# Kernel tuning notes

Measured on AMD Instinct MI355X. Metric: run time of the kernel, lower is better.

Reference implementation:

```python
import jax, jax.numpy as jnp
import numpy as np
from jax import lax

N_TAPS = 27  # 3x3x3 kernel

def _gather_one(xb, ti, hi, wi):
    # xb: (C,T,H,W); ti/hi/wi: (T,H,W) int32. Zero-fill outside bounds.
    C, T, H, W = xb.shape
    valid = (ti >= 0) & (ti < T) & (hi >= 0) & (hi < H) & (wi >= 0) & (wi < W)
    lin = (jnp.clip(ti, 0, T - 1) * H + jnp.clip(hi, 0, H - 1)) * W + jnp.clip(wi, 0, W - 1)
    v = jnp.take(xb.reshape(C, -1), lin.reshape(-1), axis=1).reshape(C, T, H, W)
    return v * valid.astype(xb.dtype)

_gather = jax.vmap(_gather_one)  # over batch

def _trilinear(x, t, h, w):
    # x: (B,C,T,H,W); t/h/w: (B,T,H,W) float sample coordinates.
    t0, h0, w0 = jnp.floor(t), jnp.floor(h), jnp.floor(w)
    lt, lh, lw = t - t0, h - h0, w - w0
    t0i, h0i, w0i = t0.astype(jnp.int32), h0.astype(jnp.int32), w0.astype(jnp.int32)
    acc = 0.0
    for ti, wt in ((t0i, 1.0 - lt), (t0i + 1, lt)):
        for hi, wh in ((h0i, 1.0 - lh), (h0i + 1, lh)):
            for wi, ww in ((w0i, 1.0 - lw), (w0i + 1, lw)):
                acc = acc + _gather(x, ti, hi, wi) * (wt * wh * ww)[:, None]
    return acc  # (B,C,T,H,W)

def _deform_conv3d(x, offset_w, offset_b, weight):
    # x: (B,Cin,T,H,W). Offset layout: (B, 3, 27, T, H, W), axis1=(dt,dh,dw),
    # tap index k = kt*9 + kh*3 + kw. stride=1, padding=1, dilation=1, no bias.
    off = lax.conv_general_dilated(
        x, offset_w, (1, 1, 1), [(1, 1)] * 3,
        dimension_numbers=("NCDHW", "OIDHW", "NCDHW"))
    off = off + offset_b[None, :, None, None, None]
    B, _, T, H, W = off.shape
    off = off.reshape(B, 3, N_TAPS, T, H, W)
    tg = jnp.arange(T, dtype=x.dtype)[:, None, None]
    hg = jnp.arange(H, dtype=x.dtype)[None, :, None]
    wg = jnp.arange(W, dtype=x.dtype)[None, None, :]
    out = jnp.zeros((B, weight.shape[0], T, H, W), x.dtype)
    for k in range(N_TAPS):
        kt, kh, kw = k // 9, (k // 3) % 3, k % 3
        t = tg + (kt - 1) + off[:, 0, k]
        h = hg + (kh - 1) + off[:, 1, k]
        w = wg + (kw - 1) + off[:, 2, k]
        s = _trilinear(x, t, h, w)  # (B,Cin,T,H,W)
        out = out + jnp.einsum('bcthw,oc->bothw', s, weight[:, :, kt, kh, kw])
    return out

def setup_inputs() -> dict:
    key = jax.random.key(0)
    ks = jax.random.split(key, 4)
    B, T, C, H, W = 1, 4, 64, 128, 128
    x = jax.random.normal(ks[0], (B, T, C, H, W), jnp.float32)
    # small init scale keeps predicted offsets in a realistic +-2px range
    offset_w = jax.random.normal(ks[1], (3 * N_TAPS, C, 3, 3, 3), jnp.float32) * 0.02
    offset_b = jnp.zeros((3 * N_TAPS,), jnp.float32)
    weight = jax.random.normal(ks[2], (C, C, 3, 3, 3), jnp.float32) * 0.02
    gamma = jax.random.normal(ks[3], (1,), jnp.float32) * 0.1
    return {"x": x, "offset_w": offset_w, "offset_b": offset_b,
            "weight": weight, "gamma": gamma}

def reference(x, offset_w, offset_b, weight, gamma):
    xp = jnp.transpose(x, (0, 2, 1, 3, 4))  # (B,C,T,H,W)
    xc = _deform_conv3d(xp, offset_w, offset_b, weight)
    return gamma[0] * jnp.transpose(xc, (0, 2, 1, 3, 4)) + x
```

## Files before the change

kernel.cpp:

```cpp
#include <hip/hip_runtime.h>
#include <cmath>

#define Cc 64
#define Hh 128
#define Ww 128
#define HW_ 16384
#define THW_ 65536
#define CHW_ 1048576
#define NT 27

typedef unsigned short ushort_t;
typedef _Float16 f16x2 __attribute__((ext_vector_type(2)));
typedef _Float16 f16x8 __attribute__((ext_vector_type(8)));
typedef __fp16 fp16x2_alt __attribute__((ext_vector_type(2)));
typedef float floatx4 __attribute__((ext_vector_type(4)));
typedef unsigned uint4v __attribute__((ext_vector_type(4)));

union U32H2 { unsigned u; f16x2 h; };

static __device__ inline ushort_t f2h(float f) {
  union { _Float16 h; ushort_t u; } v;
  v.h = (_Float16)f;
  return v.u;
}

static __device__ inline unsigned pk2(float a) {
  union { fp16x2_alt h; unsigned u; } v;
  v.h = __builtin_amdgcn_cvt_pkrtz(a, a);
  return v.u;
}

static __device__ inline unsigned rep16(unsigned p) {
#if defined(__has_builtin)
#if __has_builtin(__builtin_amdgcn_perm)
  return __builtin_amdgcn_perm(p, p, 0x01000100u);
#else
  return (p & 0xFFFFu) * 0x10001u;
#endif
#else
  return (p & 0xFFFFu) * 0x10001u;
#endif
}

#if defined(__has_builtin)
#if __has_builtin(__builtin_amdgcn_make_buffer_rsrc) && __has_builtin(__builtin_amdgcn_raw_buffer_load_b32) && __has_builtin(__builtin_amdgcn_raw_buffer_load_b128)
#define USE_BUF 1
#endif
#endif
#ifndef USE_BUF
#define USE_BUF 0
#endif

struct XtBuf {
#if USE_BUF
  __amdgpu_buffer_rsrc_t r;
#else
  const char* p;
#endif
};

static __device__ inline XtBuf mkbuf(const ushort_t* xt) {
  XtBuf b;
#if USE_BUF
  b.r = __builtin_amdgcn_make_buffer_rsrc((void*)xt, (short)0, 8388608, 0x00020000);
#else
  b.p = (const char*)xt;
#endif
  return b;
}

static __device__ inline uint4v xload4(const XtBuf& b, unsigned voff) {
#if USE_BUF
  return __builtin_amdgcn_raw_buffer_load_b128(b.r, (int)voff, 0, 0);
#else
  return *(const uint4v*)(b.p + voff);
#endif
}


__global__ __launch_bounds__(256) void prep_transpose(
    const float* __restrict__ x, ushort_t* __restrict__ xt,
    const float* __restrict__ offset_w,
    const float* __restrict__ weight,
    ushort_t* __restrict__ w2frag,
    ushort_t* __restrict__ wfrag)
{
  __shared__ float tile[64][65];
  if (blockIdx.x < 1024) {
    int b = blockIdx.x;
    int wblk = b & 1;
    int th = b >> 1;
    int h = th & 127;
    int t = th >> 7;
    int w0 = wblk * 64;
    int lane = threadIdx.x & 63;
    int quad = threadIdx.x >> 6;
    #pragma unroll
    for (int cc = 0; cc < 16; ++cc) {
      int c = cc * 4 + quad;
      tile[c][lane] = x[t * CHW_ + c * HW_ + h * Ww + w0 + lane];
    }
    __syncthreads();
    #pragma unroll
    for (int ww = 0; ww < 16; ++ww) {
      int w = ww * 4 + quad;
      xt[(size_t)(t * HW_ + h * Ww + w0 + w) * 64 + lane] = f2h(tile[lane][w]);
    }
  } else {
    int e = (blockIdx.x - 1024) * 256 + threadIdx.x;
    if (e < 165888) {
      int j = e & 7, ln = (e >> 3) & 63, kh2 = (e >> 9) & 1, r = e >> 10;
      int ot = r % 6, k = r / 6;
      int oc = ot * 16 + (ln & 15);
      int c  = kh2 * 32 + (ln >> 4) * 8 + j;
      float v = (oc < 81) ? offset_w[(oc * 64 + c) * 27 + k] : 0.f;
      w2frag[e] = f2h(v);
    }
    if (e < 110592) {
      int j = e & 7, ln = (e >> 3) & 63, kh2 = (e >> 9) & 1, r = e >> 10;
      int ot = r & 3, k = r >> 2;
      int o = ot * 16 + (ln & 15);
      int c = kh2 * 32 + (ln >> 4) * 8 + j;
      wfrag[e] = f2h(weight[(o * 64 + c) * 27 + k]);
    }
  }
}

#define SITE(W, D, A0, A1, A2, A3) \
  { U32H2 wu; wu.u = (W); U32H2 q0, q1, q2, q3; \
    q0.u = (D)[0]; q1.u = (D)[1]; q2.u = (D)[2]; q3.u = (D)[3]; \
    A0 += wu.h * q0.h; A1 += wu.h * q1.h; A2 += wu.h * q2.h; A3 += wu.h * q3.h; }

__global__ __launch_bounds__(256, 3) void fused(
    const float* __restrict__ x,
    const ushort_t* __restrict__ xt,
    const ushort_t* __restrict__ w2frag,
    const float* __restrict__ ob,
    const ushort_t* __restrict__ wfrag,
    const float* __restrict__ gamma,
    float* __restrict__ out)
{
  __shared__ __align__(16) char lds[50768];
  ushort_t* S = (ushort_t*)lds;
  unsigned* pm0 = (unsigned*)(lds + 9216);
  unsigned* pm1 = (unsigned*)(lds + 11264);
  ushort_t* W2lds = (ushort_t*)(lds + 9216);
  ushort_t* Wl0 = (ushort_t*)(lds + 13312);
  ushort_t* Wl1 = (ushort_t*)(lds + 21504);
  float* Obuf = (float*)(lds + 29696);
  float* Dbuf = (float*)lds;
  int tid = threadIdx.x;
  int lane = tid & 63;
  int wavei = __builtin_amdgcn_readfirstlane(tid >> 6);
  int quad = lane >> 4;
  int m16 = lane & 15;
  int g8 = lane >> 3;
  unsigned coff = (unsigned)((lane & 7) * 16);
  int bid0 = blockIdx.x;
  int p0 = ((bid0 & 7) * 128 + (bid0 >> 3)) * 64;
  int t = p0 >> 14;
  int h = (p0 >> 7) & 127;
  int w0 = p0 & 127;
  XtBuf xb = mkbuf(xt);

  {
    floatx4 acc[6];
    #pragma unroll
    for (int i = 0; i < 6; ++i) acc[i] = (floatx4){0.f, 0.f, 0.f, 0.f};

    uint4v pd[2];
    uint4v w2reg[3];

    auto issue = [&](int k) {
      int kt = k / 9, kh = (k / 3) % 3, kw = k % 3;
      int ts = t + kt - 1, hs = h + kh - 1;
      int tsc = min(max(ts, 0), 3);
      int hsc = min(max(hs, 0), 127);
      int sbase = tsc * HW_ + hsc * Ww;
      #pragma unroll
      for (int b = 0; b < 2; ++b) {
        int prow = wavei * 16 + b * 8 + g8;
        int wc = w0 + prow + kw - 1;
        int wcc = min(max(wc, 0), 127);
        pd[b] = xload4(xb, ((unsigned)(sbase + wcc) << 7) + coff);
      }
    };
    auto wload = [&](int k) {
      const uint4v* src = (const uint4v*)(w2frag + (size_t)k * 6144);
      #pragma unroll
      for (int c = 0; c < 3; ++c) w2reg[c] = src[tid + c * 256];
    };
    auto wstore = [&]() {
      uint4v* dst = (uint4v*)W2lds;
      #pragma unroll
      for (int c = 0; c < 3; ++c) dst[tid + c * 256] = w2reg[c];
    };

    wload(0);
    wstore();
    __syncthreads();
    issue(0);

    #pragma unroll 1
    for (int k = 0; k < NT; ++k) {
      bool more = (k + 1 < NT);
      if (more) wload(k + 1);
      __builtin_amdgcn_sched_barrier(0);
      f16x8 wva[6], wvb[6];
      #pragma unroll
      for (int ot = 0; ot < 6; ++ot) {
        wva[ot] = *(const f16x8*)(W2lds + ot * 1024 + lane * 8);
        wvb[ot] = *(const f16x8*)(W2lds + ot * 1024 + 512 + lane * 8);
      }
      int kt = k / 9, kh = (k / 3) % 3, kw = k % 3;
      int ts = t + kt - 1, hs = h + kh - 1;
      bool rowok = ((unsigned)ts < 4u) && ((unsigned)hs < 128u);
      #pragma unroll
      for (int b = 0; b < 2; ++b) {
        int prow = wavei * 16 + b * 8 + g8;
        int wc = w0 + prow + kw - 1;
        bool ok = rowok && ((unsigned)wc < 128u);
        uint4v v = pd[b];
        if (!ok) v = (uint4v){0u, 0u, 0u, 0u};
        *(uint4v*)((char*)S + prow * 144 + coff) = v;
      }
      __builtin_amdgcn_sched_barrier(0);
      const ushort_t* srow = S + (wavei * 16 + m16) * 72 + quad * 8;
      f16x8 af0 = *(const f16x8*)srow;
      f16x8 af1 = *(const f16x8*)(srow + 32);
      #pragma unroll
      for (int ot = 0; ot < 6; ++ot) {
        acc[ot] = __builtin_amdgcn_mfma_f32_16x16x32_f16(af0, wva[ot], acc[ot], 0, 0, 0);
        acc[ot] = __builtin_amdgcn_mfma_f32_16x16x32_f16(af1, wvb[ot], acc[ot], 0, 0, 0);
      }
      __syncthreads();
      if (more) wstore();
      __syncthreads();
      if (more) issue(k + 1);
    }
    #pragma unroll
    for (int ot = 0; ot < 6; ++ot) {
      int oc = ot * 16 + m16;
      if (oc < 81) {
        float bv = ob[oc];
        #pragma unroll
        for (int r = 0; r < 4; ++r)
          Obuf[oc * 65 + wavei * 16 + quad * 4 + r] = acc[ot][r] + bv;
      }
    }
  }

  floatx4 acc[4];
  #pragma unroll
  for (int i = 0; i < 4; ++i) acc[i] = (floatx4){0.f, 0.f, 0.f, 0.f};

  int pl = wavei * 16 + m16;
  int aq = quad >> 1, bq = quad & 1;
  int rowA = wavei * 16 + g8;
  int rowB = rowA + 8;

  uint4v stage[16];
  uint4v wreg[2];

  auto meta = [&](int kk, float dtv, float dhv, float dwv) {
    unsigned* pm = (kk & 1) ? pm1 : pm0;
    int kt = kk / 9, kh = (kk / 3) % 3, kw = kk % 3;
    float tf = (float)(t + kt - 1) + dtv;
    float hf = (float)(h + kh - 1) + dhv;
    float wf = (float)(w0 + pl + kw - 1) + dwv;
    float tF = floorf(tf), hF = floorf(hf), wF = floorf(wf);
    float lt = tf - tF, lh_ = hf - hF, lw_ = wf - wF;
    int t0 = (int)tF, h0 = (int)hF, wq_ = (int)wF;
    int ti = t0 + aq;
    float wt_ = (aq ? lt : 1.f - lt) * (((unsigned)ti < 4u) ? 1.f : 0.f);
    int tic = min(max(ti, 0), 3);
    int hi = h0 + bq;
    float wh_ = (bq ? lh_ : 1.f - lh_) * (((unsigned)hi < 128u) ? 1.f : 0.f);
    int hic = min(max(hi, 0), 127);
    int base2 = tic * HW_ + hic * Ww;
    float bw = wt_ * wh_;
    int wi0 = wq_;
    float ww0 = (1.f - lw_) * (((unsigned)wi0 < 128u) ? 1.f : 0.f);
    int wi0c = min(max(wi0, 0), 127);
    int wi1 = wq_ + 1;
    float ww1 = lw_ * (((unsigned)wi1 < 128u) ? 1.f : 0.f);
    int wi1c = min(max(wi1, 0), 127);
    uint2 mp_;
    mp_.x = ((unsigned)(base2 + wi0c) << 16) | (pk2(bw * ww0) & 0xFFFFu);
    mp_.y = ((unsigned)(base2 + wi1c) << 16) | (pk2(bw * ww1) & 0xFFFFu);
    *(uint2*)&pm[pl * 8 + quad * 2] = mp_;
  };

  auto vof = [&](unsigned p) -> unsigned {
    return ((p >> 9) & 0xFFFFFF80u) + coff;
  };

  auto wload2 = [&](int k) {
    const uint4v* src = (const uint4v*)(wfrag + (size_t)k * 4096);
    wreg[0] = src[tid];
    wreg[1] = src[tid + 256];
  };
  auto wstore2 = [&](int k) {
    uint4v* dst = (uint4v*)((k & 1) ? Wl1 : Wl0);
    dst[tid] = wreg[0];
    dst[tid + 256] = wreg[1];
  };

  auto issueAll = [&](int kk) {
    const unsigned* pmn = (kk & 1) ? pm1 : pm0;
    const uint4* spA = (const uint4*)&pmn[rowA * 8];
    uint4 a0 = spA[0], a1 = spA[1];
    const uint4* spB = (const uint4*)&pmn[rowB * 8];
    uint4 b0 = spB[0], b1 = spB[1];
    stage[0]  = xload4(xb, vof(a0.x));
    stage[1]  = xload4(xb, vof(a0.y));
    stage[2]  = xload4(xb, vof(a0.z));
    stage[3]  = xload4(xb, vof(a0.w));
    stage[4]  = xload4(xb, vof(a1.x));
    stage[5]  = xload4(xb, vof(a1.y));
    stage[6]  = xload4(xb, vof(a1.z));
    stage[7]  = xload4(xb, vof(a1.w));
    stage[8]  = xload4(xb, vof(b0.x));
    stage[9]  = xload4(xb, vof(b0.y));
    stage[10] = xload4(xb, vof(b0.z));
    stage[11] = xload4(xb, vof(b0.w));
    stage[12] = xload4(xb, vof(b1.x));
    stage[13] = xload4(xb, vof(b1.y));
    stage[14] = xload4(xb, vof(b1.z));
    stage[15] = xload4(xb, vof(b1.w));
  };

  auto consumeA = [&](int kk) {
    const unsigned* pmc = (kk & 1) ? pm1 : pm0;
    const uint4* wp = (const uint4*)&pmc[rowA * 8];
    uint4 w03 = wp[0], w47 = wp[1];
    U32H2 z; z.u = 0;
    f16x2 e0 = z.h, e1 = z.h, e2 = z.h, e3 = z.h;
    f16x2 o0 = z.h, o1 = z.h, o2 = z.h, o3 = z.h;
    SITE(rep16(w03.x), stage[0], e0, e1, e2, e3)
    SITE(rep16(w03.y), stage[1], o0, o1, o2, o3)
    SITE(rep16(w03.z), stage[2], e0, e1, e2, e3)
    SITE(rep16(w03.w), stage[3], o0, o1, o2, o3)
    SITE(rep16(w47.x), stage[4], e0, e1, e2, e3)
    SITE(rep16(w47.y), stage[5], o0, o1, o2, o3)
    SITE(rep16(w47.z), stage[6], e0, e1, e2, e3)
    SITE(rep16(w47.w), stage[7], o0, o1, o2, o3)
    U32H2 r0, r1, r2, r3;
    r0.h = e0 + o0; r1.h = e1 + o1; r2.h = e2 + o2; r3.h = e3 + o3;
    uint4v res = {r0.u, r1.u, r2.u, r3.u};
    *(uint4v*)((char*)S + rowA * 144 + coff) = res;
  };
  auto consumeB = [&](int kk) {
    const unsigned* pmc = (kk & 1) ? pm1 : pm0;
    const uint4* wp = (const uint4*)&pmc[rowB * 8];
    uint4 w03 = wp[0], w47 = wp[1];
    U32H2 z; z.u = 0;
    f16x2 e0 = z.h, e1 = z.h, e2 = z.h, e3 = z.h;
    f16x2 o0 = z.h, o1 = z.h, o2 = z.h, o3 = z.h;
    SITE(rep16(w03.x), stage[8],  e0, e1, e2, e3)
    SITE(rep16(w03.y), stage[9],  o0, o1, o2, o3)
    SITE(rep16(w03.z), stage[10], e0, e1, e2, e3)
    SITE(rep16(w03.w), stage[11], o0, o1, o2, o3)
    SITE(rep16(w47.x), stage[12], e0, e1, e2, e3)
    SITE(rep16(w47.y), stage[13], o0, o1, o2, o3)
    SITE(rep16(w47.z), stage[14], e0, e1, e2, e3)
    SITE(rep16(w47.w), stage[15], o0, o1, o2, o3)
    U32H2 r0, r1, r2, r3;
    r0.h = e0 + o0; r1.h = e1 + o1; r2.h = e2 + o2; r3.h = e3 + o3;
    uint4v res = {r0.u, r1.u, r2.u, r3.u};
    *(uint4v*)((char*)S + rowB * 144 + coff) = res;
  };

  __syncthreads();
  wload2(0);
  {
    float dt0 = Obuf[(0 * NT + 0) * 65 + pl];
    float dh0 = Obuf[(1 * NT + 0) * 65 + pl];
    float dw0 = Obuf[(2 * NT + 0) * 65 + pl];
    meta(0, dt0, dh0, dw0);
  }
  wstore2(0);
  __syncthreads();
  issueAll(0);

  #pragma unroll 1
  for (int k = 0; k < NT; ++k) {
    bool more = (k + 1 < NT);
    if (more) wload2(k + 1);
    if (more) {
      float dt_n = Obuf[(0 * NT + (k + 1)) * 65 + pl];
      float dh_n = Obuf[(1 * NT + (k + 1)) * 65 + pl];
      float dw_n = Obuf[(2 * NT + (k + 1)) * 65 + pl];
      meta(k + 1, dt_n, dh_n, dw_n);
    }
    __builtin_amdgcn_sched_barrier(0);
    consumeA(k);
    consumeB(k);
    __builtin_amdgcn_sched_barrier(0);
    f16x8 wva[4], wvb[4];
    {
      const ushort_t* Wl = (k & 1) ? Wl1 : Wl0;
      #pragma unroll
      for (int ot = 0; ot < 4; ++ot) {
        wva[ot] = *(const f16x8*)(Wl + ot * 1024 + lane * 8);
        wvb[ot] = *(const f16x8*)(Wl + ot * 1024 + 512 + lane * 8);
      }
    }
    if (more) wstore2(k + 1);
    const ushort_t* srow = S + (wavei * 16 + m16) * 72 + quad * 8;
    f16x8 af0 = *(const f16x8*)srow;
    f16x8 af1 = *(const f16x8*)(srow + 32);
    #pragma unroll
    for (int ot = 0; ot < 4; ++ot) {
      acc[ot] = __builtin_amdgcn_mfma_f32_16x16x32_f16(af0, wva[ot], acc[ot], 0, 0, 0);
      acc[ot] = __builtin_amdgcn_mfma_f32_16x16x32_f16(af1, wvb[ot], acc[ot], 0, 0, 0);
    }
    __syncthreads();
    if (more) issueAll(k + 1);
  }
  __syncthreads();
  #pragma unroll
  for (int ot = 0; ot < 4; ++ot)
    #pragma unroll
    for (int r = 0; r < 4; ++r)
      Dbuf[(ot * 16 + m16) * 65 + wavei * 16 + quad * 4 + r] = acc[ot][r];
  __syncthreads();
  float g = gamma[0];
  for (int i = threadIdx.x; i < 64 * 64; i += 256) {
    int oc = i >> 6, p = i & 63;
    size_t oi = (size_t)t * CHW_ + (size_t)oc * HW_ + (size_t)h * Ww + w0 + p;
    out[oi] = fmaf(g, Dbuf[oc * 65 + p], x[oi]);
  }
}

extern "C" void kernel_launch(void* const* d_in, const int* in_sizes, int n_in,
                              void* d_out, int out_size, void* d_ws, size_t ws_size,
                              hipStream_t stream) {
  (void)in_sizes; (void)n_in; (void)out_size; (void)ws_size;
  const float* x        = (const float*)d_in[0];
  const float* offset_w = (const float*)d_in[1];
  const float* offset_b = (const float*)d_in[2];
  const float* weight   = (const float*)d_in[3];
  const float* gamma    = (const float*)d_in[4];
  float* out = (float*)d_out;
  float* wsf = (float*)d_ws;
  ushort_t* xt     = (ushort_t*)(wsf + 5308416);
  ushort_t* wfrag  = (ushort_t*)(wsf + 7405568);
  ushort_t* w2frag = (ushort_t*)(wsf + 7460864);

  hipLaunchKernelGGL(prep_transpose, dim3(1672), dim3(256), 0, stream,
                     x, xt, offset_w, weight, w2frag, wfrag);
  hipLaunchKernelGGL(fused, dim3(1024), dim3(256), 0, stream,
                     x, xt, w2frag, offset_b, wfrag, gamma, out);
}
```

Measured before the change: 199.8 us.

## Vectorize prep transpose and stage weight fragment packing through LDS

The prep kernel now transposes a full 128-wide row per block, using float4 loads and 16-byte packed fp16 stores in place of scalar 2-byte stores. The offset and main weight fragment builds now read contiguous float4 chunks into LDS as fp16, then gather and write 16-byte fragments, which replaces the strided scalar global reads. This cuts the grid from 1672 to 531 blocks. It is meant to reduce prep-kernel memory-transaction overhead, at the cost of LDS bank conflicts from strided reads and fewer blocks for latency hiding.

```diff
diff --git a/kernel.cpp b/kernel.cpp
--- a/kernel.cpp
+++ b/kernel.cpp
@@ -30,6 +30,10 @@
   return v.u;
 }
 
+static __device__ inline unsigned packh2(float a, float b) {
+  return (unsigned)f2h(a) | ((unsigned)f2h(b) << 16);
+}
+
 static __device__ inline unsigned rep16(unsigned p) {
 #if defined(__has_builtin)
 #if __has_builtin(__builtin_amdgcn_perm)
@@ -85,43 +89,104 @@
     ushort_t* __restrict__ w2frag,
     ushort_t* __restrict__ wfrag)
 {
-  __shared__ float tile[64][65];
-  if (blockIdx.x < 1024) {
-    int b = blockIdx.x;
-    int wblk = b & 1;
-    int th = b >> 1;
-    int h = th & 127;
-    int t = th >> 7;
-    int w0 = wblk * 64;
-    int lane = threadIdx.x & 63;
-    int quad = threadIdx.x >> 6;
+  __shared__ __align__(16) char smem[33280];
+  int tid = threadIdx.x;
+  int b = blockIdx.x;
+  if (b < 512) {
+    float* tile = (float*)smem;
+    int t = b >> 7, h = b & 127;
+    const float* xrow = x + (size_t)t * CHW_ + (size_t)h * Ww;
+    int c0 = tid >> 5;
+    int w4 = (tid & 31) * 4;
     #pragma unroll
-    for (int cc = 0; cc < 16; ++cc) {
-      int c = cc * 4 + quad;
-      tile[c][lane] = x[t * CHW_ + c * HW_ + h * Ww + w0 + lane];
+    for (int p = 0; p < 8; ++p) {
+      int c = p * 8 + c0;
+      float4 v = *(const float4*)(xrow + (size_t)c * HW_ + w4);
+      tile[(w4 + 0) * 65 + c] = v.x;
+      tile[(w4 + 1) * 65 + c] = v.y;
+      tile[(w4 + 2) * 65 + c] = v.z;
+      tile[(w4 + 3) * 65 + c] = v.w;
     }
     __syncthreads();
+    int oct = tid & 7;
+    int pbase = tid >> 3;
+    ushort_t* xrowo = xt + (size_t)(t * HW_ + h * Ww) * 64;
     #pragma unroll
-    for (int ww = 0; ww < 16; ++ww) {
-      int w = ww * 4 + quad;
-      xt[(size_t)(t * HW_ + h * Ww + w0 + w) * 64 + lane] = f2h(tile[lane][w]);
+    for (int p = 0; p < 4; ++p) {
+      int pos = p * 32 + pbase;
+      const float* src = &tile[pos * 65 + oct * 8];
+      uint4 u;
+      u.x = packh2(src[0], src[1]);
+      u.y = packh2(src[2], src[3]);
+      u.z = packh2(src[4], src[5]);
+      u.w = packh2(src[6], src[7]);
+      *(uint4*)(xrowo + (size_t)pos * 64 + oct * 8) = u;
+    }
+  } else if (b < 523) {
+    ushort_t* ldsw = (ushort_t*)smem;
+    int i = b - 512;
+    const float* src = offset_w + (size_t)i * 13824;
+    int limit = 139968 - i * 13824;
+    for (int idx = tid * 4; idx < 13824; idx += 1024) {
+      float4 v = make_float4(0.f, 0.f, 0.f, 0.f);
+      if (idx < limit) v = *(const float4*)(src + idx);
+      ldsw[idx + 0] = f2h(v.x);
+      ldsw[idx + 1] = f2h(v.y);
+      ldsw[idx + 2] = f2h(v.z);
+      ldsw[idx + 3] = f2h(v.w);
+    }
+    __syncthreads();
+    int ot = i >> 1;
+    int lnlo = (i & 1) * 8;
+    for (int ch = tid; ch < 1728; ch += 256) {
+      int lnsub = ch & 7;
+      int lnhi = (ch >> 3) & 3;
+      int kh2 = (ch >> 5) & 1;
+      int k = ch >> 6;
+      int ln = lnhi * 16 + lnlo + lnsub;
+      uint4 u;
+      unsigned uu[4];
+      #pragma unroll
+      for (int q = 0; q < 4; ++q) {
+        int c0 = kh2 * 32 + lnhi * 8 + 2 * q;
+        ushort_t a = ldsw[lnsub * 1728 + c0 * 27 + k];
+        ushort_t bb = ldsw[lnsub * 1728 + (c0 + 1) * 27 + k];
+        uu[q] = (unsigned)a | ((unsigned)bb << 16);
+      }
+      u.x = uu[0]; u.y = uu[1]; u.z = uu[2]; u.w = uu[3];
+      *(uint4*)(w2frag + (size_t)(((k * 6 + ot) * 2 + kh2) * 512 + ln * 8)) = u;
     }
   } else {
-    int e = (blockIdx.x - 1024) * 256 + threadIdx.x;
-    if (e < 165888) {
-      int j = e & 7, ln = (e >> 3) & 63, kh2 = (e >> 9) & 1, r = e >> 10;
-      int ot = r % 6, k = r / 6;
-      int oc = ot * 16 + (ln & 15);
-      int c  = kh2 * 32 + (ln >> 4) * 8 + j;
-      float v = (oc < 81) ? offset_w[(oc * 64 + c) * 27 + k] : 0.f;
-      w2frag[e] = f2h(v);
-    }
-    if (e < 110592) {
-      int j = e & 7, ln = (e >> 3) & 63, kh2 = (e >> 9) & 1, r = e >> 10;
-      int ot = r & 3, k = r >> 2;
-      int o = ot * 16 + (ln & 15);
-      int c = kh2 * 32 + (ln >> 4) * 8 + j;
-      wfrag[e] = f2h(weight[(o * 64 + c) * 27 + k]);
+    ushort_t* ldsw = (ushort_t*)smem;
+    int i = b - 523;
+    const float* src = weight + (size_t)i * 13824;
+    for (int idx = tid * 4; idx < 13824; idx += 1024) {
+      float4 v = *(const float4*)(src + idx);
+      ldsw[idx + 0] = f2h(v.x);
+      ldsw[idx + 1] = f2h(v.y);
+      ldsw[idx + 2] = f2h(v.z);
+      ldsw[idx + 3] = f2h(v.w);
+    }
+    __syncthreads();
+    int ot = i >> 1;
+    int lnlo = (i & 1) * 8;
+    for (int ch = tid; ch < 1728; ch += 256) {
+      int lnsub = ch & 7;
+      int lnhi = (ch >> 3) & 3;
+      int kh2 = (ch >> 5) & 1;
+      int k = ch >> 6;
+      int ln = lnhi * 16 + lnlo + lnsub;
+      uint4 u;
+      unsigned uu[4];
+      #pragma unroll
+      for (int q = 0; q < 4; ++q) {
+        int c0 = kh2 * 32 + lnhi * 8 + 2 * q;
+        ushort_t a = ldsw[lnsub * 1728 + c0 * 27 + k];
+        ushort_t bb = ldsw[lnsub * 1728 + (c0 + 1) * 27 + k];
+        uu[q] = (unsigned)a | ((unsigned)bb << 16);
+      }
+      u.x = uu[0]; u.y = uu[1]; u.z = uu[2]; u.w = uu[3];
+      *(uint4*)(wfrag + (size_t)(((k * 4 + ot) * 2 + kh2) * 512 + ln * 8)) = u;
     }
   }
 }
@@ -448,7 +513,7 @@
   ushort_t* wfrag  = (ushort_t*)(wsf + 7405568);
   ushort_t* w2frag = (ushort_t*)(wsf + 7460864);
 
-  hipLaunchKernelGGL(prep_transpose, dim3(1672), dim3(256), 0, stream,
+  hipLaunchKernelGGL(prep_transpose, dim3(531), dim3(256), 0, stream,
                      x, xt, offset_w, weight, w2frag, wfrag);
   hipLaunchKernelGGL(fused, dim3(1024), dim3(256), 0, stream,
                      x, xt, w2frag, offset_b, wfrag, gamma, out);
```

New measurement: 204.4 us. 1.02x slower.
